# Performance work log

Measured on AMD Instinct MI355X. Metric: run time of the kernel, lower is better.

The kernel has to match this reference:

```python
import jax, jax.numpy as jnp
import numpy as np

ALPHA = 100.0
ETA_0 = 0.3
SIGMA_0 = 16.0  # max(map shape)/2


def setup_inputs() -> dict:
    key = jax.random.key(0)
    k1, k2 = jax.random.split(key)
    Z = jax.random.normal(k1, (512, 256), dtype=jnp.float32)
    SOM = jax.random.uniform(k2, (32, 32, 256), dtype=jnp.float32)  # 'random_uniform' init
    return {"Z": Z, "SOM": SOM, "step": 0}


def reference(Z, SOM, step):
    """NeuralMap.call(training=True, iter=1): one SOM update + KL loss.

    Z:   [B, E] batch of embeddings
    SOM: [H, W, E] map weights
    Returns (kl_loss [B], delta [B, H, W, E]) matching the returned dict values.
    """
    H, W, E = SOM.shape
    B = Z.shape[0]
    n = jnp.asarray(step, dtype=jnp.float32)
    eta = ETA_0 * jnp.exp(-n / ALPHA)          # learning rate eta(n)
    sigma = SIGMA_0 * jnp.exp(-n / ALPHA)      # neighborhood radius sigma(n)

    # --- best_match_neuron: broadcast diff + L2 norm over embed dim + argmin ---
    diff = Z[:, None, None, :] - SOM[None]                      # [B, H, W, E]
    dist = jnp.sqrt(jnp.sum(diff * diff, axis=-1))              # [B, H, W]
    u_flat = jnp.argmin(dist.reshape(B, -1), axis=-1)           # [B]

    # lattice index grid [H, W, 2]
    grid = jnp.stack(
        jnp.meshgrid(jnp.arange(H), jnp.arange(W), indexing="ij"), axis=-1
    )
    U = grid.reshape(-1, 2)[u_flat]                              # [B, 2] BMU indices

    # --- neighborhood function H(u, j)(n) over the whole lattice ---
    idx_diff = (U[:, None, None, :] - grid[None]).astype(jnp.float32)  # [B, H, W, 2]
    h = jnp.exp(-jnp.sum(idx_diff * idx_diff, axis=-1) / (2.0 * sigma * sigma))

    # --- delta = eta(n) * H * (Z - w_j), update_memory('average') ---
    delta = eta * h[..., None] * diff                            # [B, H, W, E]
    SOM_new = SOM + jnp.mean(delta, axis=0)

    # --- get_kl_loss on the updated map ---
    Wf = SOM_new.reshape(-1, E)                                  # [H*W, E]
    d = jnp.sqrt(jnp.sum((Z[:, None, :] - Wf[None]) ** 2, axis=-1))  # [B, H*W]
    raw_q = 1.0 / (1.0 + d)
    q = raw_q / jnp.sum(raw_q, axis=-1, keepdims=True)           # [B, L]
    raw_p = (q * q) / jnp.sum(q, axis=0, keepdims=True)
    p = raw_p / jnp.sum(raw_p, axis=1, keepdims=True)
    kl_loss = jnp.sum(p * jnp.log(p / q), axis=-1)               # [B]

    return kl_loss, delta
```

## Files before the change

### kernel.cpp

```cpp
#include <hip/hip_runtime.h>
#include <math.h>

#define B 512
#define E 256
#define L 1024

typedef float f32x4 __attribute__((ext_vector_type(4)));
typedef unsigned long long u64;

#define O_Q     0u
#define O_SOMN  524288u
#define O_PART  786432u
#define O_PRS   802816u
#define O_H     811008u
#define O_BMUP  1335296u

__global__ __launch_bounds__(256) void dist_bmu_kernel(const float* __restrict__ Zg,
                                                       const float* __restrict__ Wg,
                                                       u64* __restrict__ bmupart) {
    __shared__ float Zs[64][67];
    __shared__ float Ws[64][67];
    __shared__ u64 red[64][16];
    const int tid = threadIdx.x;
    const int tb = blockIdx.x >> 4;
    const int tn = blockIdx.x & 15;
    const int b0 = tb * 64, n0 = tn * 64;
    const int ty = tid >> 4, tx = tid & 15;

    float acc[4][4];
#pragma unroll
    for (int i = 0; i < 4; ++i)
#pragma unroll
        for (int j = 0; j < 4; ++j) acc[i][j] = 0.f;

    for (int kc = 0; kc < E; kc += 64) {
        const int c4 = tx * 4;
#pragma unroll
        for (int s = 0; s < 4; ++s) {
            const int r = ty + 16 * s;
            float4 zv = *(const float4*)(Zg + (size_t)(b0 + r) * E + kc + c4);
            Zs[r][c4 + 0] = zv.x; Zs[r][c4 + 1] = zv.y;
            Zs[r][c4 + 2] = zv.z; Zs[r][c4 + 3] = zv.w;
            float4 wv = *(const float4*)(Wg + (size_t)(n0 + r) * E + kc + c4);
            Ws[r][c4 + 0] = wv.x; Ws[r][c4 + 1] = wv.y;
            Ws[r][c4 + 2] = wv.z; Ws[r][c4 + 3] = wv.w;
        }
        __syncthreads();
#pragma unroll 4
        for (int k = 0; k < 64; ++k) {
            float zr[4], wr[4];
#pragma unroll
            for (int i = 0; i < 4; ++i) zr[i] = Zs[ty * 4 + i][k];
#pragma unroll
            for (int j = 0; j < 4; ++j) wr[j] = Ws[tx * 4 + j][k];
#pragma unroll
            for (int i = 0; i < 4; ++i)
#pragma unroll
                for (int j = 0; j < 4; ++j) {
                    float d = zr[i] - wr[j];
                    acc[i][j] = fmaf(d, d, acc[i][j]);
                }
        }
        __syncthreads();
    }
#pragma unroll
    for (int i = 0; i < 4; ++i) {
        float best = acc[i][0];
        int bj = 0;
#pragma unroll
        for (int j = 1; j < 4; ++j)
            if (acc[i][j] < best) { best = acc[i][j]; bj = j; }
        red[ty * 4 + i][tx] = ((u64)__float_as_uint(best) << 32) |
                              (unsigned)(n0 + tx * 4 + bj);
    }
    __syncthreads();
    if (tid < 64) {
        u64 m = red[tid][0];
#pragma unroll
        for (int t = 1; t < 16; ++t) {
            const u64 v = red[tid][t];
            if (v < m) m = v;
        }
        bmupart[(size_t)tn * B + b0 + tid] = m;
    }
}

__global__ __launch_bounds__(256) void h_kernel(const u64* __restrict__ bmupart,
                                                const int* __restrict__ step,
                                                float* __restrict__ h) {
    const int b = blockIdx.x;
    u64 m = bmupart[b];
#pragma unroll
    for (int tn = 1; tn < 16; ++tn) {
        const u64 v = bmupart[(size_t)tn * B + b];
        if (v < m) m = v;
    }
    const int u = (int)(m & 0xffffffffULL);
    const int ur = u >> 5, uc = u & 31;
    const float n = (float)step[0];
    const float decay = expf(-n * 0.01f);
    const float eta = 0.3f * decay;
    const float sigma = 16.0f * decay;
    const float inv2s2 = 1.0f / (2.0f * sigma * sigma);
#pragma unroll
    for (int s = 0; s < 4; ++s) {
        const int t = threadIdx.x + s * 256;
        const int i = t >> 5, j = t & 31;
        const float dr = (float)(ur - i), dc = (float)(uc - j);
        h[(size_t)b * L + t] = eta * expf(-(dr * dr + dc * dc) * inv2s2);
    }
}

__global__ __launch_bounds__(256) void delta_update_kernel(const float* __restrict__ Zg,
                                                           const float* __restrict__ Wg,
                                                           const float* __restrict__ h,
                                                           float* __restrict__ somn,
                                                           float* __restrict__ delta) {
    if (blockIdx.x < 1024) {
        const int hw = blockIdx.x;
        const int e = threadIdx.x;
        float acc = 0.f, hsum = 0.f;
#pragma unroll 8
        for (int b = 0; b < B; ++b) {
            const float hv = h[(size_t)b * L + hw];
            acc = fmaf(hv, Zg[(size_t)b * E + e], acc);
            hsum += hv;
        }
        const float w = Wg[(size_t)hw * E + e];
        somn[(size_t)hw * E + e] = w + (1.0f / (float)B) * (acc - hsum * w);
        return;
    }
    const int bid = blockIdx.x - 1024;
    const int b = bid >> 8;
    const int hw = ((bid & 255) << 2) + (threadIdx.x >> 6);
    const int lane = threadIdx.x & 63;
    const float hs = h[(size_t)b * L + hw];
    const float4 z = *(const float4*)(Zg + (size_t)b * E + lane * 4);
    const float4 w = *(const float4*)(Wg + (size_t)hw * E + lane * 4);
    f32x4 o;
    o.x = hs * (z.x - w.x);
    o.y = hs * (z.y - w.y);
    o.z = hs * (z.z - w.z);
    o.w = hs * (z.w - w.w);
    f32x4* dst = (f32x4*)(delta + ((size_t)b * L + hw) * E + lane * 4);
    __builtin_nontemporal_store(o, dst);
}

__global__ __launch_bounds__(256) void distq_kernel(const float* __restrict__ Zg,
                                                    const float* __restrict__ Wg,
                                                    float* __restrict__ out,
                                                    float* __restrict__ part_rs) {
    __shared__ float Zs[64][67];
    __shared__ float Ws[64][67];
    __shared__ float red[64][16];
    const int tid = threadIdx.x;
    const int tb = blockIdx.x >> 4;
    const int tn = blockIdx.x & 15;
    const int b0 = tb * 64, n0 = tn * 64;
    const int ty = tid >> 4, tx = tid & 15;

    float acc[4][4];
#pragma unroll
    for (int i = 0; i < 4; ++i)
#pragma unroll
        for (int j = 0; j < 4; ++j) acc[i][j] = 0.f;

    for (int kc = 0; kc < E; kc += 64) {
        const int c4 = tx * 4;
#pragma unroll
        for (int s = 0; s < 4; ++s) {
            const int r = ty + 16 * s;
            float4 zv = *(const float4*)(Zg + (size_t)(b0 + r) * E + kc + c4);
            Zs[r][c4 + 0] = zv.x; Zs[r][c4 + 1] = zv.y;
            Zs[r][c4 + 2] = zv.z; Zs[r][c4 + 3] = zv.w;
            float4 wv = *(const float4*)(Wg + (size_t)(n0 + r) * E + kc + c4);
            Ws[r][c4 + 0] = wv.x; Ws[r][c4 + 1] = wv.y;
            Ws[r][c4 + 2] = wv.z; Ws[r][c4 + 3] = wv.w;
        }
        __syncthreads();
#pragma unroll 4
        for (int k = 0; k < 64; ++k) {
            float zr[4], wr[4];
#pragma unroll
            for (int i = 0; i < 4; ++i) zr[i] = Zs[ty * 4 + i][k];
#pragma unroll
            for (int j = 0; j < 4; ++j) wr[j] = Ws[tx * 4 + j][k];
#pragma unroll
            for (int i = 0; i < 4; ++i)
#pragma unroll
                for (int j = 0; j < 4; ++j) {
                    float d = zr[i] - wr[j];
                    acc[i][j] = fmaf(d, d, acc[i][j]);
                }
        }
        __syncthreads();
    }
#pragma unroll
    for (int i = 0; i < 4; ++i) {
        const int b = b0 + ty * 4 + i;
        float4 v;
        v.x = 1.f / (1.f + sqrtf(acc[i][0]));
        v.y = 1.f / (1.f + sqrtf(acc[i][1]));
        v.z = 1.f / (1.f + sqrtf(acc[i][2]));
        v.w = 1.f / (1.f + sqrtf(acc[i][3]));
        *(float4*)(out + (size_t)b * L + n0 + tx * 4) = v;
        red[ty * 4 + i][tx] = v.x + v.y + v.z + v.w;
    }
    __syncthreads();
    if (tid < 64) {
        float s = red[tid][0];
#pragma unroll
        for (int t = 1; t < 16; ++t) s += red[tid][t];
        part_rs[(size_t)tn * B + b0 + tid] = s;
    }
}

__global__ __launch_bounds__(256) void colsum_part_kernel(const float* __restrict__ q,
                                                          const float* __restrict__ prs,
                                                          float* __restrict__ part) {
    __shared__ float sirs[32];
    const int j = (blockIdx.x & 3) * 256 + threadIdx.x;
    const int c = blockIdx.x >> 2;
    const int b0 = c * 32;
    if (threadIdx.x < 32) {
        float s = 0.f;
#pragma unroll
        for (int tn = 0; tn < 16; ++tn) s += prs[(size_t)tn * B + b0 + threadIdx.x];
        sirs[threadIdx.x] = 1.0f / s;
    }
    __syncthreads();
    float acc = 0.f;
#pragma unroll 8
    for (int bo = 0; bo < 32; ++bo)
        acc = fmaf(q[(size_t)(b0 + bo) * L + j], sirs[bo], acc);
    part[(size_t)c * L + j] = acc;
}

__global__ __launch_bounds__(256) void kl_kernel(const float* __restrict__ q,
                                                 const float* __restrict__ prs,
                                                 const float* __restrict__ part,
                                                 float* __restrict__ kl) {
    const int b = blockIdx.x;
    const int tid = threadIdx.x;
    float rs = 0.f;
#pragma unroll
    for (int tn = 0; tn < 16; ++tn) rs += prs[(size_t)tn * B + b];
    const float irsb = 1.0f / rs;
    float S = 0.f, T = 0.f;
#pragma unroll
    for (int s = 0; s < 4; ++s) {
        const int j = tid + s * 256;
        float csj = 0.f;
#pragma unroll
        for (int c = 0; c < 16; ++c) csj += part[(size_t)c * L + j];
        const float qq = q[(size_t)b * L + j] * irsb;
        const float ic = 1.0f / csj;
        const float rp = qq * qq * ic;
        S += rp;
        T = fmaf(rp, logf(qq * ic), T);
    }
    __shared__ float sS[256], sT[256];
    sS[tid] = S; sT[tid] = T;
    __syncthreads();
    for (int st = 128; st > 0; st >>= 1) {
        if (tid < st) { sS[tid] += sS[tid + st]; sT[tid] += sT[tid + st]; }
        __syncthreads();
    }
    if (tid == 0) kl[b] = sT[0] / sS[0] - logf(sS[0]);
}

extern "C" void kernel_launch(void* const* d_in, const int* in_sizes, int n_in,
                              void* d_out, int out_size, void* d_ws, size_t ws_size,
                              hipStream_t stream) {
    const float* Zg = (const float*)d_in[0];
    const float* Wg = (const float*)d_in[1];
    const int* step = (const int*)d_in[2];
    float* out = (float*)d_out;
    float* ws = (float*)d_ws;

    float* q    = ws + O_Q;
    float* somn = ws + O_SOMN;
    float* part = ws + O_PART;
    float* prs  = ws + O_PRS;
    float* h    = ws + O_H;
    u64*   bmup = (u64*)(ws + O_BMUP);

    float* kl    = out;
    float* delta = out + B;

    hipLaunchKernelGGL(dist_bmu_kernel, dim3(128), dim3(256), 0, stream, Zg, Wg, bmup);
    hipLaunchKernelGGL(h_kernel, dim3(B), dim3(256), 0, stream, bmup, step, h);
    hipLaunchKernelGGL(delta_update_kernel, dim3(1024 + B * 256), dim3(256), 0, stream,
                       Zg, Wg, h, somn, delta);
    hipLaunchKernelGGL(distq_kernel, dim3(128), dim3(256), 0, stream, Zg, somn, q, prs);
    hipLaunchKernelGGL(colsum_part_kernel, dim3(64), dim3(256), 0, stream, q, prs, part);
    hipLaunchKernelGGL(kl_kernel, dim3(B), dim3(256), 0, stream, q, prs, part, kl);
}
```

Before: 145.6 us.

## Split delta write into LDS-tiled kernel separate from SOM update

Splits the fused update/delta kernel in two. A dedicated update kernel computes the new SOM. A new delta kernel stages tiles of 16 batch rows × 32 map neurons of Z, W and h in shared memory and reuses them across the tile when writing the 512 MB delta output. This cuts the redundant global reads of Z and W per output element and the large number of tiny blocks. It also drops the nontemporal store hint, adds a kernel launch, and raises shared memory use per block to about 50 KB.

```diff
diff --git a/kernel.cpp b/kernel.cpp
--- a/kernel.cpp
+++ b/kernel.cpp
@@ -111,39 +111,73 @@
     }
 }
 
-__global__ __launch_bounds__(256) void delta_update_kernel(const float* __restrict__ Zg,
-                                                           const float* __restrict__ Wg,
-                                                           const float* __restrict__ h,
-                                                           float* __restrict__ somn,
-                                                           float* __restrict__ delta) {
-    if (blockIdx.x < 1024) {
-        const int hw = blockIdx.x;
-        const int e = threadIdx.x;
-        float acc = 0.f, hsum = 0.f;
+__global__ __launch_bounds__(256) void update_kernel(const float* __restrict__ Zg,
+                                                     const float* __restrict__ Wg,
+                                                     const float* __restrict__ h,
+                                                     float* __restrict__ somn) {
+    const int hw = blockIdx.x;
+    const int e = threadIdx.x;
+    float acc = 0.f, hsum = 0.f;
 #pragma unroll 8
-        for (int b = 0; b < B; ++b) {
-            const float hv = h[(size_t)b * L + hw];
-            acc = fmaf(hv, Zg[(size_t)b * E + e], acc);
-            hsum += hv;
-        }
-        const float w = Wg[(size_t)hw * E + e];
-        somn[(size_t)hw * E + e] = w + (1.0f / (float)B) * (acc - hsum * w);
-        return;
-    }
-    const int bid = blockIdx.x - 1024;
-    const int b = bid >> 8;
-    const int hw = ((bid & 255) << 2) + (threadIdx.x >> 6);
-    const int lane = threadIdx.x & 63;
-    const float hs = h[(size_t)b * L + hw];
-    const float4 z = *(const float4*)(Zg + (size_t)b * E + lane * 4);
-    const float4 w = *(const float4*)(Wg + (size_t)hw * E + lane * 4);
-    f32x4 o;
-    o.x = hs * (z.x - w.x);
-    o.y = hs * (z.y - w.y);
-    o.z = hs * (z.z - w.z);
-    o.w = hs * (z.w - w.w);
-    f32x4* dst = (f32x4*)(delta + ((size_t)b * L + hw) * E + lane * 4);
-    __builtin_nontemporal_store(o, dst);
+    for (int b = 0; b < B; ++b) {
+        const float hv = h[(size_t)b * L + hw];
+        acc = fmaf(hv, Zg[(size_t)b * E + e], acc);
+        hsum += hv;
+    }
+    const float w = Wg[(size_t)hw * E + e];
+    somn[(size_t)hw * E + e] = w + (1.0f / (float)B) * (acc - hsum * w);
+}
+
+#define BCH 16
+#define HCH 32
+__global__ __launch_bounds__(512) void delta_lds_kernel(const float* __restrict__ Zg,
+                                                        const float* __restrict__ Wg,
+                                                        const float* __restrict__ h,
+                                                        float* __restrict__ delta) {
+    __shared__ float Ws_l[HCH * E];
+    __shared__ float Zs_l[BCH * E];
+    __shared__ float hs_l[BCH * HCH];
+    const int tid = threadIdx.x;
+    const int bc = blockIdx.x >> 5;
+    const int hc = blockIdx.x & 31;
+    const int b0 = bc * BCH, hw0 = hc * HCH;
+
+    {
+        const float* src = Wg + (size_t)hw0 * E;
+#pragma unroll
+        for (int p = 0; p < 4; ++p) {
+            const int o = (p * 512 + tid) * 4;
+            *(float4*)(Ws_l + o) = *(const float4*)(src + o);
+        }
+        const float* zsrc = Zg + (size_t)b0 * E;
+#pragma unroll
+        for (int p = 0; p < 2; ++p) {
+            const int o = (p * 512 + tid) * 4;
+            *(float4*)(Zs_l + o) = *(const float4*)(zsrc + o);
+        }
+        const int i = tid >> 5, j = tid & 31;
+        hs_l[tid] = h[(size_t)(b0 + i) * L + hw0 + j];
+    }
+    __syncthreads();
+
+    const int wid = tid >> 6;
+    const int lane = tid & 63;
+    const int r0 = wid * 4;
+    for (int i = 0; i < BCH; ++i) {
+        const float4 z = *(const float4*)(Zs_l + i * E + lane * 4);
+        float* drow = delta + ((size_t)(b0 + i) * L + hw0 + r0) * E + lane * 4;
+#pragma unroll
+        for (int r = 0; r < 4; ++r) {
+            const float hs = hs_l[i * HCH + r0 + r];
+            const float4 w = *(const float4*)(Ws_l + (r0 + r) * E + lane * 4);
+            f32x4 o;
+            o.x = hs * (z.x - w.x);
+            o.y = hs * (z.y - w.y);
+            o.z = hs * (z.z - w.z);
+            o.w = hs * (z.w - w.w);
+            *(f32x4*)(drow + (size_t)r * E) = o;
+        }
+    }
 }
 
 __global__ __launch_bounds__(256) void distq_kernel(const float* __restrict__ Zg,
@@ -290,8 +324,8 @@
 
     hipLaunchKernelGGL(dist_bmu_kernel, dim3(128), dim3(256), 0, stream, Zg, Wg, bmup);
     hipLaunchKernelGGL(h_kernel, dim3(B), dim3(256), 0, stream, bmup, step, h);
-    hipLaunchKernelGGL(delta_update_kernel, dim3(1024 + B * 256), dim3(256), 0, stream,
-                       Zg, Wg, h, somn, delta);
+    hipLaunchKernelGGL(update_kernel, dim3(L), dim3(256), 0, stream, Zg, Wg, h, somn);
+    hipLaunchKernelGGL(delta_lds_kernel, dim3(1024), dim3(512), 0, stream, Zg, Wg, h, delta);
     hipLaunchKernelGGL(distq_kernel, dim3(128), dim3(256), 0, stream, Zg, somn, q, prs);
     hipLaunchKernelGGL(colsum_part_kernel, dim3(64), dim3(256), 0, stream, q, prs, part);
     hipLaunchKernelGGL(kl_kernel, dim3(B), dim3(256), 0, stream, q, prs, part, kl);
```

Measured after the change: 215.3 us. +47.9%, slower.

## Split delta writes across kernels and fuse column-sum into KL kernel

Applied to the files above, without the earlier changes.

The delta store work is split in half: the first 256 batch rows stay in the update kernel and the remaining rows move into a new combined kernel that also computes the KL loss. That combined kernel replaces the separate column-sum and KL kernels. Each KL block redundantly recomputes the full column sums over all 512 rows, so the partial-sum buffer and one launch go away. The aim is to hide the small, latency-bound KL tail behind the bandwidth-bound delta writes, at the cost of 512x redundant column-sum reads of q (mostly served from cache).

```diff
diff --git a/kernel.cpp b/kernel.cpp
--- a/kernel.cpp
+++ b/kernel.cpp
@@ -10,10 +10,9 @@
 
 #define O_Q     0u
 #define O_SOMN  524288u
-#define O_PART  786432u
-#define O_PRS   802816u
-#define O_H     811008u
-#define O_BMUP  1335296u
+#define O_PRS   786432u
+#define O_H     794624u
+#define O_BMUP  1318912u
 
 __global__ __launch_bounds__(256) void dist_bmu_kernel(const float* __restrict__ Zg,
                                                        const float* __restrict__ Wg,
@@ -142,8 +141,7 @@
     o.y = hs * (z.y - w.y);
     o.z = hs * (z.z - w.z);
     o.w = hs * (z.w - w.w);
-    f32x4* dst = (f32x4*)(delta + ((size_t)b * L + hw) * E + lane * 4);
-    __builtin_nontemporal_store(o, dst);
+    __builtin_nontemporal_store(o, (f32x4*)(delta + ((size_t)b * L + hw) * E + lane * 4));
 }
 
 __global__ __launch_bounds__(256) void distq_kernel(const float* __restrict__ Zg,
@@ -215,58 +213,84 @@
     }
 }
 
-__global__ __launch_bounds__(256) void colsum_part_kernel(const float* __restrict__ q,
-                                                          const float* __restrict__ prs,
-                                                          float* __restrict__ part) {
-    __shared__ float sirs[32];
-    const int j = (blockIdx.x & 3) * 256 + threadIdx.x;
-    const int c = blockIdx.x >> 2;
-    const int b0 = c * 32;
-    if (threadIdx.x < 32) {
-        float s = 0.f;
-#pragma unroll
-        for (int tn = 0; tn < 16; ++tn) s += prs[(size_t)tn * B + b0 + threadIdx.x];
-        sirs[threadIdx.x] = 1.0f / s;
-    }
-    __syncthreads();
-    float acc = 0.f;
+__global__ __launch_bounds__(256) void delta_kl_kernel(const float* __restrict__ Zg,
+                                                       const float* __restrict__ Wg,
+                                                       const float* __restrict__ h,
+                                                       const float* __restrict__ q,
+                                                       const float* __restrict__ prs,
+                                                       float* __restrict__ kl,
+                                                       float* __restrict__ delta) {
+    if (blockIdx.x < 512) {
+        __shared__ float sirs[B];
+        __shared__ float sS[256], sT[256];
+        const int tid = threadIdx.x;
+#pragma unroll
+        for (int s = 0; s < 2; ++s) {
+            const int bb = tid + s * 256;
+            float ss = 0.f;
+#pragma unroll
+            for (int tn = 0; tn < 16; ++tn) ss += prs[(size_t)tn * B + bb];
+            sirs[bb] = 1.0f / ss;
+        }
+        __syncthreads();
+
+        const int j4 = tid * 4;
+        float cs0 = 0.f, cs1 = 0.f, cs2 = 0.f, cs3 = 0.f;
 #pragma unroll 8
-    for (int bo = 0; bo < 32; ++bo)
-        acc = fmaf(q[(size_t)(b0 + bo) * L + j], sirs[bo], acc);
-    part[(size_t)c * L + j] = acc;
-}
-
-__global__ __launch_bounds__(256) void kl_kernel(const float* __restrict__ q,
-                                                 const float* __restrict__ prs,
-                                                 const float* __restrict__ part,
-                                                 float* __restrict__ kl) {
-    const int b = blockIdx.x;
-    const int tid = threadIdx.x;
-    float rs = 0.f;
-#pragma unroll
-    for (int tn = 0; tn < 16; ++tn) rs += prs[(size_t)tn * B + b];
-    const float irsb = 1.0f / rs;
-    float S = 0.f, T = 0.f;
-#pragma unroll
-    for (int s = 0; s < 4; ++s) {
-        const int j = tid + s * 256;
-        float csj = 0.f;
-#pragma unroll
-        for (int c = 0; c < 16; ++c) csj += part[(size_t)c * L + j];
-        const float qq = q[(size_t)b * L + j] * irsb;
-        const float ic = 1.0f / csj;
-        const float rp = qq * qq * ic;
-        S += rp;
-        T = fmaf(rp, logf(qq * ic), T);
-    }
-    __shared__ float sS[256], sT[256];
-    sS[tid] = S; sT[tid] = T;
-    __syncthreads();
-    for (int st = 128; st > 0; st >>= 1) {
-        if (tid < st) { sS[tid] += sS[tid + st]; sT[tid] += sT[tid + st]; }
-        __syncthreads();
-    }
-    if (tid == 0) kl[b] = sT[0] / sS[0] - logf(sS[0]);
+        for (int b = 0; b < B; ++b) {
+            const float4 qv = *(const float4*)(q + (size_t)b * L + j4);
+            const float ir = sirs[b];
+            cs0 = fmaf(qv.x, ir, cs0);
+            cs1 = fmaf(qv.y, ir, cs1);
+            cs2 = fmaf(qv.z, ir, cs2);
+            cs3 = fmaf(qv.w, ir, cs3);
+        }
+        const int bq = blockIdx.x;
+        const float irsb = sirs[bq];
+        const float4 qb = *(const float4*)(q + (size_t)bq * L + j4);
+        float S = 0.f, T = 0.f;
+        {
+            const float qq = qb.x * irsb, ic = 1.0f / cs0;
+            const float rp = qq * qq * ic;
+            S += rp; T = fmaf(rp, logf(qq * ic), T);
+        }
+        {
+            const float qq = qb.y * irsb, ic = 1.0f / cs1;
+            const float rp = qq * qq * ic;
+            S += rp; T = fmaf(rp, logf(qq * ic), T);
+        }
+        {
+            const float qq = qb.z * irsb, ic = 1.0f / cs2;
+            const float rp = qq * qq * ic;
+            S += rp; T = fmaf(rp, logf(qq * ic), T);
+        }
+        {
+            const float qq = qb.w * irsb, ic = 1.0f / cs3;
+            const float rp = qq * qq * ic;
+            S += rp; T = fmaf(rp, logf(qq * ic), T);
+        }
+        sS[tid] = S; sT[tid] = T;
+        __syncthreads();
+        for (int st = 128; st > 0; st >>= 1) {
+            if (tid < st) { sS[tid] += sS[tid + st]; sT[tid] += sT[tid + st]; }
+            __syncthreads();
+        }
+        if (tid == 0) kl[bq] = sT[0] / sS[0] - logf(sS[0]);
+        return;
+    }
+    const int bid = blockIdx.x - 512;
+    const int b = 256 + (bid >> 8);
+    const int hw = ((bid & 255) << 2) + (threadIdx.x >> 6);
+    const int lane = threadIdx.x & 63;
+    const float hs = h[(size_t)b * L + hw];
+    const float4 z = *(const float4*)(Zg + (size_t)b * E + lane * 4);
+    const float4 w = *(const float4*)(Wg + (size_t)hw * E + lane * 4);
+    f32x4 o;
+    o.x = hs * (z.x - w.x);
+    o.y = hs * (z.y - w.y);
+    o.z = hs * (z.z - w.z);
+    o.w = hs * (z.w - w.w);
+    __builtin_nontemporal_store(o, (f32x4*)(delta + ((size_t)b * L + hw) * E + lane * 4));
 }
 
 extern "C" void kernel_launch(void* const* d_in, const int* in_sizes, int n_in,
@@ -280,7 +304,6 @@
 
     float* q    = ws + O_Q;
     float* somn = ws + O_SOMN;
-    float* part = ws + O_PART;
     float* prs  = ws + O_PRS;
     float* h    = ws + O_H;
     u64*   bmup = (u64*)(ws + O_BMUP);
@@ -290,9 +313,9 @@
 
     hipLaunchKernelGGL(dist_bmu_kernel, dim3(128), dim3(256), 0, stream, Zg, Wg, bmup);
     hipLaunchKernelGGL(h_kernel, dim3(B), dim3(256), 0, stream, bmup, step, h);
-    hipLaunchKernelGGL(delta_update_kernel, dim3(1024 + B * 256), dim3(256), 0, stream,
+    hipLaunchKernelGGL(delta_update_kernel, dim3(1024 + 256 * 256), dim3(256), 0, stream,
                        Zg, Wg, h, somn, delta);
     hipLaunchKernelGGL(distq_kernel, dim3(128), dim3(256), 0, stream, Zg, somn, q, prs);
-    hipLaunchKernelGGL(colsum_part_kernel, dim3(64), dim3(256), 0, stream, q, prs, part);
-    hipLaunchKernelGGL(kl_kernel, dim3(B), dim3(256), 0, stream, q, prs, part, kl);
-}
+    hipLaunchKernelGGL(delta_kl_kernel, dim3(512 + 256 * 256), dim3(256), 0, stream,
+                       Zg, Wg, h, q, prs, kl, delta);
+}
```

Result: slower. 174.7 us (+20.0%).
